# Performance work log

Measured on AMD Instinct MI355X. Metric: run time of the kernel, lower is better.

## Reference

```python
import jax, jax.numpy as jnp
import numpy as np

B, ES, HS, NL, NOUT, T = 16384, 64, 64, 3, 2, 128


def setup_inputs() -> dict:
    key = jax.random.key(0)
    ks = jax.random.split(key, 9)
    k = 1.0 / np.sqrt(HS)
    u = lambda kk, shape: jax.random.uniform(kk, shape, jnp.float32, -k, k)
    return {
        "agentFutureTrajEnc": jax.random.normal(ks[0], (B, ES), jnp.float32),
        "emb_w": u(ks[1], (ES, ES)),
        "emb_b": u(ks[2], (ES,)),
        "w_ih": u(ks[3], (NL, 3 * HS, ES)),
        "w_hh": u(ks[4], (NL, 3 * HS, HS)),
        "b_ih": u(ks[5], (NL, 3 * HS)),
        "b_hh": u(ks[6], (NL, 3 * HS)),
        "out_w": u(ks[7], (NOUT, HS)),
        "out_b": u(ks[8], (NOUT,)),
        "target_length": T,
        "batch_size": B,
    }


def _gru_cell(x, h, Wi, Wh, bi, bh):
    # PyTorch GRU cell math: gates ordered (r, z, n)
    gi = x @ Wi.T + bi            # (B, 3*hs)
    gh = h @ Wh.T + bh            # (B, 3*hs)
    ir, iz, inn = jnp.split(gi, 3, axis=-1)
    hr, hz, hn = jnp.split(gh, 3, axis=-1)
    r = jax.nn.sigmoid(ir + hr)
    z = jax.nn.sigmoid(iz + hz)
    n = jnp.tanh(inn + r * hn)
    return (1.0 - z) * n + z * h


def reference(agentFutureTrajEnc, emb_w, emb_b, w_ih, w_hh, b_ih, b_hh, out_w, out_b,
              target_length, batch_size):
    nl = w_ih.shape[0]
    # hidden initialized by repeating the encoding across layers: (nl, B, hs)
    h0 = jnp.broadcast_to(agentFutureTrajEnc[None], (nl,) + agentFutureTrajEnc.shape)

    def step(carry, _):
        x, h = carry                      # x: (B, es), h: (nl, B, hs)
        inp = x @ emb_w.T + emb_b         # embedding Linear(es->es)
        new_h = []
        for l in range(nl):               # small fixed layer loop
            hl = _gru_cell(inp, h[l], w_ih[l], w_hh[l], b_ih[l], b_hh[l])
            new_h.append(hl)
            inp = hl
        h = jnp.stack(new_h)              # (nl, B, hs)
        out = inp @ out_w.T + out_b       # (B, nout)
        return (h[-1], h), out            # next input is top-layer hidden

    _, outs = jax.lax.scan(step, (agentFutureTrajEnc, h0), None, length=target_length)
    return jnp.transpose(outs, (1, 0, 2))  # (B, T, nout)
```

## Files before the change

kernel.cpp:

```cpp
#include <hip/hip_runtime.h>


#define ESZ   64
#define HSZ   64
#define TLEN  128
#define NOUTC 2
#define LDW   72
#define TB16  (16*LDW)
#define L2E   1.44269504f

typedef _Float16 half8 __attribute__((ext_vector_type(8)));
typedef _Float16 half4 __attribute__((ext_vector_type(4)));
typedef float    floatx4 __attribute__((ext_vector_type(4)));
typedef float    floatx2 __attribute__((ext_vector_type(2)));

#define MFMA(a, b, c) __builtin_amdgcn_mfma_f32_16x16x32_f16((a), (b), (c), 0, 0, 0)

#define SBAR() asm volatile("s_waitcnt lgkmcnt(0)\n\ts_barrier" ::: "memory")

__global__ __launch_bounds__(768, 3) void gru_pipe(
    const float* __restrict__ enc,
    const float* __restrict__ emb_w,
    const float* __restrict__ emb_b,
    const float* __restrict__ w_ih,
    const float* __restrict__ w_hh,
    const float* __restrict__ b_ih,
    const float* __restrict__ b_hh,
    const float* __restrict__ out_w,
    const float* __restrict__ out_b,
    float* __restrict__ out)
{
    __shared__ _Float16 s_hl[3 * 2 * 2 * TB16];
    __shared__ float    s_btmp[3 * 64];

    const int tid  = threadIdx.x;
    const int wave = tid >> 6, lane = tid & 63;
    const int l = wave >> 2, g = wave & 3;
    const int q = lane >> 4, c = lane & 15;
    const int u  = (g << 4) | c;
    const int u4 = (g << 4) | (q << 2);
    const long wgbase = (long)blockIdx.x * 32;

    if (tid < 256) {
        const int row = tid >> 3, k0 = (tid & 7) << 3;
        const int j = row >> 4, rr = row & 15;
        const float* p = enc + (wgbase + row) * ESZ + k0;
        floatx4 s0 = *(const floatx4*)p;
        floatx4 s1 = *(const floatx4*)(p + 4);
        half8 v;
        #pragma unroll
        for (int x = 0; x < 4; ++x) { v[x] = (_Float16)s0[x]; v[4 + x] = (_Float16)s1[x]; }
        #pragma unroll
        for (int ly = 0; ly < 3; ++ly)
            *(half8*)&s_hl[((ly * 2 + j) * 2 + 1) * TB16 + rr * LDW + k0] = v;
    }

    auto ldw8s = [&](const float* p, float sc) {
        floatx4 a = *(const floatx4*)p, b = *(const floatx4*)(p + 4);
        half8 v;
        #pragma unroll
        for (int x = 0; x < 4; ++x) { v[x] = (_Float16)(a[x] * sc); v[4 + x] = (_Float16)(b[x] * sc); }
        return v;
    };
    half8 fR[4], fZ[4], fNi[2], fNh[2], fO[2];
    fO[0] = fO[1] = half8{};
    if (l == 0) {
        const float* wi = w_ih;
        const float* wh = w_hh;
        floatx4 aR[4], aZ[4], aN[4];
        #pragma unroll
        for (int x = 0; x < 4; ++x) { aR[x] = {0,0,0,0}; aZ[x] = {0,0,0,0}; aN[x] = {0,0,0,0}; }
        float bR = 0.f, bZ = 0.f, bN = 0.f;
        for (int k4 = 0; k4 < 64; k4 += 4) {
            floatx4 wr4 = *(const floatx4*)(wi + (u) * 64 + k4);
            floatx4 wz4 = *(const floatx4*)(wi + (64 + u) * 64 + k4);
            floatx4 wn4 = *(const floatx4*)(wi + (128 + u) * 64 + k4);
            floatx4 be4 = *(const floatx4*)(emb_b + k4);
            #pragma unroll
            for (int kk = 0; kk < 4; ++kk) {
                const float* er = emb_w + (k4 + kk) * 64;
                floatx4 e0 = *(const floatx4*)(er + q * 8);
                floatx4 e1 = *(const floatx4*)(er + q * 8 + 4);
                floatx4 e2 = *(const floatx4*)(er + 32 + q * 8);
                floatx4 e3 = *(const floatx4*)(er + 32 + q * 8 + 4);
                const float wr = wr4[kk], wz = wz4[kk], wn = wn4[kk];
                aR[0] += wr * e0; aR[1] += wr * e1; aR[2] += wr * e2; aR[3] += wr * e3;
                aZ[0] += wz * e0; aZ[1] += wz * e1; aZ[2] += wz * e2; aZ[3] += wz * e3;
                aN[0] += wn * e0; aN[1] += wn * e1; aN[2] += wn * e2; aN[3] += wn * e3;
                bR += wr * be4[kk]; bZ += wz * be4[kk]; bN += wn * be4[kk];
            }
        }
        #pragma unroll
        for (int x = 0; x < 4; ++x) {
            fR[0][x] = (_Float16)(-L2E * aR[0][x]);   fR[0][4 + x] = (_Float16)(-L2E * aR[1][x]);
            fR[1][x] = (_Float16)(-L2E * aR[2][x]);   fR[1][4 + x] = (_Float16)(-L2E * aR[3][x]);
            fZ[0][x] = (_Float16)(-L2E * aZ[0][x]);   fZ[0][4 + x] = (_Float16)(-L2E * aZ[1][x]);
            fZ[1][x] = (_Float16)(-L2E * aZ[2][x]);   fZ[1][4 + x] = (_Float16)(-L2E * aZ[3][x]);
            fNi[0][x] = (_Float16)(2*L2E * aN[0][x]); fNi[0][4 + x] = (_Float16)(2*L2E * aN[1][x]);
            fNi[1][x] = (_Float16)(2*L2E * aN[2][x]); fNi[1][4 + x] = (_Float16)(2*L2E * aN[3][x]);
        }
        fR[2]  = ldw8s(wh + (u) * 64 + q * 8, -L2E);        fR[3]  = ldw8s(wh + (u) * 64 + 32 + q * 8, -L2E);
        fZ[2]  = ldw8s(wh + (64 + u) * 64 + q * 8, -L2E);   fZ[3]  = ldw8s(wh + (64 + u) * 64 + 32 + q * 8, -L2E);
        fNh[0] = ldw8s(wh + (128 + u) * 64 + q * 8, 2*L2E); fNh[1] = ldw8s(wh + (128 + u) * 64 + 32 + q * 8, 2*L2E);
        if (q == 0) {
            s_btmp[u] = bR; s_btmp[64 + u] = bZ; s_btmp[128 + u] = bN;
        }
        const int oc = (c < NOUTC) ? c : 0;
        fO[0] = ldw8s(out_w + oc * 64 + q * 8, 1.f);
        fO[1] = ldw8s(out_w + oc * 64 + 32 + q * 8, 1.f);
    } else {
        const float* wi = w_ih + l * 3 * HSZ * ESZ;
        const float* wh = w_hh + l * 3 * HSZ * ESZ;
        fR[0]  = ldw8s(wi + (u) * 64 + q * 8, -L2E);        fR[1]  = ldw8s(wi + (u) * 64 + 32 + q * 8, -L2E);
        fR[2]  = ldw8s(wh + (u) * 64 + q * 8, -L2E);        fR[3]  = ldw8s(wh + (u) * 64 + 32 + q * 8, -L2E);
        fZ[0]  = ldw8s(wi + (64 + u) * 64 + q * 8, -L2E);   fZ[1]  = ldw8s(wi + (64 + u) * 64 + 32 + q * 8, -L2E);
        fZ[2]  = ldw8s(wh + (64 + u) * 64 + q * 8, -L2E);   fZ[3]  = ldw8s(wh + (64 + u) * 64 + 32 + q * 8, -L2E);
        fNi[0] = ldw8s(wi + (128 + u) * 64 + q * 8, 2*L2E); fNi[1] = ldw8s(wi + (128 + u) * 64 + 32 + q * 8, 2*L2E);
        fNh[0] = ldw8s(wh + (128 + u) * 64 + q * 8, 2*L2E); fNh[1] = ldw8s(wh + (128 + u) * 64 + 32 + q * 8, 2*L2E);
    }
    __syncthreads();

    floatx4 bR4, bZ4, bNi4, bNh4;
    if (l == 0) {
        #pragma unroll
        for (int i = 0; i < 4; ++i) {
            bR4[i]  = -L2E * (s_btmp[u4 + i] + b_ih[u4 + i] + b_hh[u4 + i]);
            bZ4[i]  = -L2E * (s_btmp[64 + u4 + i] + b_ih[64 + u4 + i] + b_hh[64 + u4 + i]);
            bNi4[i] = 2.f * L2E * (s_btmp[128 + u4 + i] + b_ih[128 + u4 + i]);
            bNh4[i] = 2.f * L2E * b_hh[128 + u4 + i];
        }
    } else {
        const int b0 = l * 192;
        floatx4 bi0 = *(const floatx4*)(b_ih + b0 + u4),       bh0 = *(const floatx4*)(b_hh + b0 + u4);
        floatx4 bi1 = *(const floatx4*)(b_ih + b0 + 64 + u4),  bh1 = *(const floatx4*)(b_hh + b0 + 64 + u4);
        floatx4 bi2 = *(const floatx4*)(b_ih + b0 + 128 + u4), bh2 = *(const floatx4*)(b_hh + b0 + 128 + u4);
        #pragma unroll
        for (int i = 0; i < 4; ++i) {
            bR4[i]  = -L2E * (bi0[i] + bh0[i]);
            bZ4[i]  = -L2E * (bi1[i] + bh1[i]);
            bNi4[i] = 2.f * L2E * bi2[i];
            bNh4[i] = 2.f * L2E * bh2[i];
        }
    }
    const float ob0 = out_b[0], ob1 = out_b[1];

    floatx4 ca0 = *(const floatx4*)(enc + (wgbase +  0 + c) * 64 + u4);
    floatx4 ca1 = *(const floatx4*)(enc + (wgbase + 16 + c) * 64 + u4);

    const int ar = c * LDW + (q << 3);

    auto visit = [&](const int ll, const int j, floatx4& cs, const int t,
                     const int parw) {
        const _Float16* hb = s_hl + ((ll * 2 + j) * 2 + (parw ^ 1)) * TB16;
        const _Float16* xb = (ll == 0) ? s_hl + ((4 + j) * 2 + (parw ^ 1)) * TB16
                                       : s_hl + (((ll - 1) * 2 + j) * 2 + parw) * TB16;
        half8 ah0 = *(const half8*)(hb + ar);
        half8 ah1 = *(const half8*)(hb + ar + 32);
        half8 bx0 = *(const half8*)(xb + ar);
        half8 bx1 = *(const half8*)(xb + ar + 32);
        floatx4 accr = bR4, accz = bZ4, accnh = bNh4;
        accr  = MFMA(fR[2], ah0, accr);   accr  = MFMA(fR[3], ah1, accr);
        accz  = MFMA(fZ[2], ah0, accz);   accz  = MFMA(fZ[3], ah1, accz);
        accnh = MFMA(fNh[0], ah0, accnh); accnh = MFMA(fNh[1], ah1, accnh);
        accr = MFMA(fR[0], bx0, accr); accr = MFMA(fR[1], bx1, accr);
        accz = MFMA(fZ[0], bx0, accz); accz = MFMA(fZ[1], bx1, accz);
        floatx4 accni = bNi4;
        accni = MFMA(fNi[0], bx0, accni); accni = MFMA(fNi[1], bx1, accni);
        _Float16* hw = s_hl + ((ll * 2 + j) * 2 + parw) * TB16 + c * LDW + u4;
        half4 hv4; floatx4 hnew;
        #pragma unroll
        for (int i = 0; i < 4; ++i) {
            const float er = __builtin_amdgcn_exp2f(accr[i]);
            const float ez = __builtin_amdgcn_exp2f(accz[i]);
            const float pr = 1.f + er, pz = 1.f + ez;
            const float qq = __builtin_amdgcn_rcpf(pr * pz);
            const float rr = qq * pz;
            const float zz = qq * pr;
            const float a  = accni[i] + rr * accnh[i];
            const float n  = 1.f - 2.f * __builtin_amdgcn_rcpf(1.f + __builtin_amdgcn_exp2f(a));
            const float hv = n + zz * (cs[i] - n);
            hnew[i] = hv; hv4[i] = (_Float16)hv;
        }
        *(half4*)hw = hv4;
        cs = hnew;
    };

    auto visO = [&](const int j, const int t, const int par) {
        const _Float16* xb = s_hl + ((4 + j) * 2 + par) * TB16;
        half8 b0 = *(const half8*)(xb + ar);
        half8 b1 = *(const half8*)(xb + ar + 32);
        floatx4 oa = {ob0, ob1, 0.f, 0.f};
        oa = MFMA(fO[0], b0, oa);
        oa = MFMA(fO[1], b1, oa);
        if (q == 0) {
            const long row = wgbase + j * 16 + c;
            *(floatx2*)(out + (row * TLEN + t) * NOUTC) = floatx2{oa[0], oa[1]};
        }
    };

    for (int t = 0; t < TLEN; t += 2) {
        const bool vv = (t != 0);
        if (l == 0)      visit(0, 0, ca0, t, 0);
        else if (l == 2) { if (vv) visit(2, 1, ca1, t - 1, 1); }
        SBAR();
        if (l == 0)      visit(0, 1, ca1, t, 0);
        else if (l == 1) visit(1, 0, ca0, t, 0);
        SBAR();
        if (l == 0)      { if (vv && g < 2) visO(g, t - 1, 1); }
        else if (l == 1) visit(1, 1, ca1, t, 0);
        else             visit(2, 0, ca0, t, 0);
        SBAR();
        if (l == 0)      visit(0, 0, ca0, t + 1, 1);
        else if (l == 2) visit(2, 1, ca1, t, 0);
        SBAR();
        if (l == 0)      visit(0, 1, ca1, t + 1, 1);
        else if (l == 1) visit(1, 0, ca0, t + 1, 1);
        SBAR();
        if (l == 0)      { if (g < 2) visO(g, t, 0); }
        else if (l == 1) visit(1, 1, ca1, t + 1, 1);
        else             visit(2, 0, ca0, t + 1, 1);
        SBAR();
    }

    if (l == 2)           visit(2, 1, ca1, TLEN - 1, 1);
    else if (l == 0 && g == 0) visO(0, TLEN - 1, 1);
    SBAR();
    if (l == 0 && g == 1) visO(1, TLEN - 1, 1);
}

extern "C" void kernel_launch(void* const* d_in, const int* in_sizes, int n_in,
                              void* d_out, int out_size, void* d_ws, size_t ws_size,
                              hipStream_t stream) {
    (void)in_sizes; (void)n_in; (void)d_ws; (void)ws_size; (void)out_size;
    const int grid = 16384 / 32;
    gru_pipe<<<grid, 768, 0, stream>>>(
        (const float*)d_in[0],
        (const float*)d_in[1],
        (const float*)d_in[2],
        (const float*)d_in[3],
        (const float*)d_in[4],
        (const float*)d_in[5],
        (const float*)d_in[6],
        (const float*)d_in[7],
        (const float*)d_in[8],
        (float*)d_out);
}
```

Baseline: 547.3 us.

## Double rows per workgroup with four tiles and a rebalanced layer pipeline schedule

Each workgroup now handles 64 batch rows as four 16-row tiles instead of 32 rows as two. The wavefront pipeline over the three layers is rescheduled so each phase processes either one tile or a paired tile (visit2), whose MFMA chains are interleaved to hide latency. The output projection is spread across more waves. This halves the grid to 256 workgroups, which may leave compute units idle on a large GPU, and it doubles LDS use.

```diff
diff --git a/kernel.cpp b/kernel.cpp
--- a/kernel.cpp
+++ b/kernel.cpp
@@ -30,7 +30,7 @@
     const float* __restrict__ out_b,
     float* __restrict__ out)
 {
-    __shared__ _Float16 s_hl[3 * 2 * 2 * TB16];
+    __shared__ _Float16 s_hl[3 * 4 * 2 * TB16];
     __shared__ float    s_btmp[3 * 64];
 
     const int tid  = threadIdx.x;
@@ -39,9 +39,9 @@
     const int q = lane >> 4, c = lane & 15;
     const int u  = (g << 4) | c;
     const int u4 = (g << 4) | (q << 2);
-    const long wgbase = (long)blockIdx.x * 32;
-
-    if (tid < 256) {
+    const long wgbase = (long)blockIdx.x * 64;
+
+    if (tid < 512) {
         const int row = tid >> 3, k0 = (tid & 7) << 3;
         const int j = row >> 4, rr = row & 15;
         const float* p = enc + (wgbase + row) * ESZ + k0;
@@ -52,7 +52,7 @@
         for (int x = 0; x < 4; ++x) { v[x] = (_Float16)s0[x]; v[4 + x] = (_Float16)s1[x]; }
         #pragma unroll
         for (int ly = 0; ly < 3; ++ly)
-            *(half8*)&s_hl[((ly * 2 + j) * 2 + 1) * TB16 + rr * LDW + k0] = v;
+            *(half8*)&s_hl[((ly * 4 + j) * 2 + 1) * TB16 + rr * LDW + k0] = v;
     }
 
     auto ldw8s = [&](const float* p, float sc) {
@@ -146,14 +146,36 @@
 
     floatx4 ca0 = *(const floatx4*)(enc + (wgbase +  0 + c) * 64 + u4);
     floatx4 ca1 = *(const floatx4*)(enc + (wgbase + 16 + c) * 64 + u4);
+    floatx4 ca2 = *(const floatx4*)(enc + (wgbase + 32 + c) * 64 + u4);
+    floatx4 ca3 = *(const floatx4*)(enc + (wgbase + 48 + c) * 64 + u4);
 
     const int ar = c * LDW + (q << 3);
+
+    auto gates = [&](floatx4& accr, floatx4& accz, floatx4& accni, floatx4& accnh,
+                     floatx4& cs, _Float16* hw) {
+        half4 hv4; floatx4 hnew;
+        #pragma unroll
+        for (int i = 0; i < 4; ++i) {
+            const float er = __builtin_amdgcn_exp2f(accr[i]);
+            const float ez = __builtin_amdgcn_exp2f(accz[i]);
+            const float pr = 1.f + er, pz = 1.f + ez;
+            const float qq = __builtin_amdgcn_rcpf(pr * pz);
+            const float rr = qq * pz;
+            const float zz = qq * pr;
+            const float a  = accni[i] + rr * accnh[i];
+            const float n  = 1.f - 2.f * __builtin_amdgcn_rcpf(1.f + __builtin_amdgcn_exp2f(a));
+            const float hv = n + zz * (cs[i] - n);
+            hnew[i] = hv; hv4[i] = (_Float16)hv;
+        }
+        *(half4*)hw = hv4;
+        cs = hnew;
+    };
 
     auto visit = [&](const int ll, const int j, floatx4& cs, const int t,
                      const int parw) {
-        const _Float16* hb = s_hl + ((ll * 2 + j) * 2 + (parw ^ 1)) * TB16;
-        const _Float16* xb = (ll == 0) ? s_hl + ((4 + j) * 2 + (parw ^ 1)) * TB16
-                                       : s_hl + (((ll - 1) * 2 + j) * 2 + parw) * TB16;
+        const _Float16* hb = s_hl + ((ll * 4 + j) * 2 + (parw ^ 1)) * TB16;
+        const _Float16* xb = (ll == 0) ? s_hl + ((8 + j) * 2 + (parw ^ 1)) * TB16
+                                       : s_hl + (((ll - 1) * 4 + j) * 2 + parw) * TB16;
         half8 ah0 = *(const half8*)(hb + ar);
         half8 ah1 = *(const half8*)(hb + ar + 32);
         half8 bx0 = *(const half8*)(xb + ar);
@@ -166,27 +188,45 @@
         accz = MFMA(fZ[0], bx0, accz); accz = MFMA(fZ[1], bx1, accz);
         floatx4 accni = bNi4;
         accni = MFMA(fNi[0], bx0, accni); accni = MFMA(fNi[1], bx1, accni);
-        _Float16* hw = s_hl + ((ll * 2 + j) * 2 + parw) * TB16 + c * LDW + u4;
-        half4 hv4; floatx4 hnew;
-        #pragma unroll
-        for (int i = 0; i < 4; ++i) {
-            const float er = __builtin_amdgcn_exp2f(accr[i]);
-            const float ez = __builtin_amdgcn_exp2f(accz[i]);
-            const float pr = 1.f + er, pz = 1.f + ez;
-            const float qq = __builtin_amdgcn_rcpf(pr * pz);
-            const float rr = qq * pz;
-            const float zz = qq * pr;
-            const float a  = accni[i] + rr * accnh[i];
-            const float n  = 1.f - 2.f * __builtin_amdgcn_rcpf(1.f + __builtin_amdgcn_exp2f(a));
-            const float hv = n + zz * (cs[i] - n);
-            hnew[i] = hv; hv4[i] = (_Float16)hv;
-        }
-        *(half4*)hw = hv4;
-        cs = hnew;
+        _Float16* hw = s_hl + ((ll * 4 + j) * 2 + parw) * TB16 + c * LDW + u4;
+        gates(accr, accz, accni, accnh, cs, hw);
+    };
+
+    auto visit2 = [&](const int ll, const int ja, floatx4& csa,
+                      const int jb, floatx4& csb, const int t, const int parw) {
+        const _Float16* hbA = s_hl + ((ll * 4 + ja) * 2 + (parw ^ 1)) * TB16;
+        const _Float16* hbB = s_hl + ((ll * 4 + jb) * 2 + (parw ^ 1)) * TB16;
+        const _Float16* xbA = (ll == 0) ? s_hl + ((8 + ja) * 2 + (parw ^ 1)) * TB16
+                                        : s_hl + (((ll - 1) * 4 + ja) * 2 + parw) * TB16;
+        const _Float16* xbB = (ll == 0) ? s_hl + ((8 + jb) * 2 + (parw ^ 1)) * TB16
+                                        : s_hl + (((ll - 1) * 4 + jb) * 2 + parw) * TB16;
+        half8 ahA0 = *(const half8*)(hbA + ar), ahA1 = *(const half8*)(hbA + ar + 32);
+        half8 bxA0 = *(const half8*)(xbA + ar), bxA1 = *(const half8*)(xbA + ar + 32);
+        half8 ahB0 = *(const half8*)(hbB + ar), ahB1 = *(const half8*)(hbB + ar + 32);
+        half8 bxB0 = *(const half8*)(xbB + ar), bxB1 = *(const half8*)(xbB + ar + 32);
+        floatx4 accrA = bR4, acczA = bZ4, accnhA = bNh4;
+        floatx4 accrB = bR4, acczB = bZ4, accnhB = bNh4;
+        accrA  = MFMA(fR[2], ahA0, accrA);   accrA  = MFMA(fR[3], ahA1, accrA);
+        accrB  = MFMA(fR[2], ahB0, accrB);   accrB  = MFMA(fR[3], ahB1, accrB);
+        acczA  = MFMA(fZ[2], ahA0, acczA);   acczA  = MFMA(fZ[3], ahA1, acczA);
+        acczB  = MFMA(fZ[2], ahB0, acczB);   acczB  = MFMA(fZ[3], ahB1, acczB);
+        accnhA = MFMA(fNh[0], ahA0, accnhA); accnhA = MFMA(fNh[1], ahA1, accnhA);
+        accnhB = MFMA(fNh[0], ahB0, accnhB); accnhB = MFMA(fNh[1], ahB1, accnhB);
+        accrA = MFMA(fR[0], bxA0, accrA); accrA = MFMA(fR[1], bxA1, accrA);
+        accrB = MFMA(fR[0], bxB0, accrB); accrB = MFMA(fR[1], bxB1, accrB);
+        acczA = MFMA(fZ[0], bxA0, acczA); acczA = MFMA(fZ[1], bxA1, acczA);
+        acczB = MFMA(fZ[0], bxB0, acczB); acczB = MFMA(fZ[1], bxB1, acczB);
+        floatx4 accniA = bNi4, accniB = bNi4;
+        accniA = MFMA(fNi[0], bxA0, accniA); accniA = MFMA(fNi[1], bxA1, accniA);
+        accniB = MFMA(fNi[0], bxB0, accniB); accniB = MFMA(fNi[1], bxB1, accniB);
+        _Float16* hwA = s_hl + ((ll * 4 + ja) * 2 + parw) * TB16 + c * LDW + u4;
+        _Float16* hwB = s_hl + ((ll * 4 + jb) * 2 + parw) * TB16 + c * LDW + u4;
+        gates(accrA, acczA, accniA, accnhA, csa, hwA);
+        gates(accrB, acczB, accniB, accnhB, csb, hwB);
     };
 
     auto visO = [&](const int j, const int t, const int par) {
-        const _Float16* xb = s_hl + ((4 + j) * 2 + par) * TB16;
+        const _Float16* xb = s_hl + ((8 + j) * 2 + par) * TB16;
         half8 b0 = *(const half8*)(xb + ar);
         half8 b1 = *(const half8*)(xb + ar + 32);
         floatx4 oa = {ob0, ob1, 0.f, 0.f};
@@ -200,39 +240,62 @@
 
     for (int t = 0; t < TLEN; t += 2) {
         const bool vv = (t != 0);
-        if (l == 0)      visit(0, 0, ca0, t, 0);
-        else if (l == 2) { if (vv) visit(2, 1, ca1, t - 1, 1); }
-        SBAR();
-        if (l == 0)      visit(0, 1, ca1, t, 0);
-        else if (l == 1) visit(1, 0, ca0, t, 0);
-        SBAR();
-        if (l == 0)      { if (vv && g < 2) visO(g, t - 1, 1); }
-        else if (l == 1) visit(1, 1, ca1, t, 0);
-        else             visit(2, 0, ca0, t, 0);
-        SBAR();
-        if (l == 0)      visit(0, 0, ca0, t + 1, 1);
-        else if (l == 2) visit(2, 1, ca1, t, 0);
-        SBAR();
-        if (l == 0)      visit(0, 1, ca1, t + 1, 1);
-        else if (l == 1) visit(1, 0, ca0, t + 1, 1);
-        SBAR();
-        if (l == 0)      { if (g < 2) visO(g, t, 0); }
-        else if (l == 1) visit(1, 1, ca1, t + 1, 1);
-        else             visit(2, 0, ca0, t + 1, 1);
+        if (l == 0) {
+            visit2(0, 0, ca0, 3, ca3, t, 0);
+            if (vv && g == 0) visO(0, t - 1, 1);
+            else if (vv && g == 3) visO(3, t - 1, 1);
+        } else if (l == 1) { if (vv) visit(1, 2, ca2, t - 1, 1); }
+        else               { if (vv) visit(2, 1, ca1, t - 1, 1); }
+        SBAR();
+        if (l == 0) {
+            visit(0, 1, ca1, t, 0);
+            if (vv && g == 1) visO(1, t - 1, 1);
+        } else if (l == 1) visit2(1, 0, ca0, 3, ca3, t, 0);
+        else               { if (vv) visit(2, 2, ca2, t - 1, 1); }
+        SBAR();
+        if (l == 0) {
+            visit(0, 2, ca2, t, 0);
+            if (vv && g == 2) visO(2, t - 1, 1);
+        } else if (l == 1) visit(1, 1, ca1, t, 0);
+        else               visit2(2, 0, ca0, 3, ca3, t, 0);
+        SBAR();
+        if (l == 0) {
+            visit2(0, 0, ca0, 3, ca3, t + 1, 1);
+            if (g == 0) visO(0, t, 0);
+            else if (g == 3) visO(3, t, 0);
+        } else if (l == 1) visit(1, 2, ca2, t, 0);
+        else               visit(2, 1, ca1, t, 0);
+        SBAR();
+        if (l == 0) {
+            visit(0, 1, ca1, t + 1, 1);
+            if (g == 1) visO(1, t, 0);
+        } else if (l == 1) visit2(1, 0, ca0, 3, ca3, t + 1, 1);
+        else               visit(2, 2, ca2, t, 0);
+        SBAR();
+        if (l == 0) {
+            visit(0, 2, ca2, t + 1, 1);
+            if (g == 2) visO(2, t, 0);
+        } else if (l == 1) visit(1, 1, ca1, t + 1, 1);
+        else               visit2(2, 0, ca0, 3, ca3, t + 1, 1);
         SBAR();
     }
 
-    if (l == 2)           visit(2, 1, ca1, TLEN - 1, 1);
+    if (l == 1)                visit(1, 2, ca2, TLEN - 1, 1);
+    else if (l == 2)           visit(2, 1, ca1, TLEN - 1, 1);
     else if (l == 0 && g == 0) visO(0, TLEN - 1, 1);
+    else if (l == 0 && g == 3) visO(3, TLEN - 1, 1);
     SBAR();
-    if (l == 0 && g == 1) visO(1, TLEN - 1, 1);
+    if (l == 2)                visit(2, 2, ca2, TLEN - 1, 1);
+    else if (l == 0 && g == 1) visO(1, TLEN - 1, 1);
+    SBAR();
+    if (l == 0 && g == 2)      visO(2, TLEN - 1, 1);
 }
 
 extern "C" void kernel_launch(void* const* d_in, const int* in_sizes, int n_in,
                               void* d_out, int out_size, void* d_ws, size_t ws_size,
                               hipStream_t stream) {
     (void)in_sizes; (void)n_in; (void)d_ws; (void)ws_size; (void)out_size;
-    const int grid = 16384 / 32;
+    const int grid = 16384 / 64;
     gru_pipe<<<grid, 768, 0, stream>>>(
         (const float*)d_in[0],
         (const float*)d_in[1],
```

Measured after the change: 460.7 us. 1.19x faster.
